# Kernel optimization log

Hardware: AMD Instinct MI355X
Metric: run time of the kernel (lower is better)

Reference implementation:

```python
import jax, jax.numpy as jnp
import numpy as np

N, E = 100000, 1600000
IN, HID, NCLS = 128, 128, 64


def setup_inputs() -> dict:
    key = jax.random.key(0)
    ks = jax.random.split(key, 8)
    x = jax.random.normal(ks[0], (N, IN), jnp.float32)
    edge_index = jax.random.randint(ks[1], (2, E), 0, N, dtype=jnp.int32)
    s1 = 1.0 / np.sqrt(IN)
    s2 = 1.0 / np.sqrt(HID)
    return {
        "x": x,
        "edge_index": edge_index,
        "Wl1": jax.random.uniform(ks[2], (IN, HID), jnp.float32, -s1, s1),
        "Wr1": jax.random.uniform(ks[3], (IN, HID), jnp.float32, -s1, s1),
        "b1": jnp.zeros((HID,), jnp.float32),
        "Wl2": jax.random.uniform(ks[4], (HID, NCLS), jnp.float32, -s2, s2),
        "Wr2": jax.random.uniform(ks[5], (HID, NCLS), jnp.float32, -s2, s2),
        "b2": jnp.zeros((NCLS,), jnp.float32),
    }


def _sage_conv(x, src, dst, inv_deg, Wl, Wr, b):
    # mean-aggregate neighbor features at each destination node (PyG SAGEConv)
    agg = jax.ops.segment_sum(x[src], dst, num_segments=N)  # [N, d]
    agg = agg * inv_deg[:, None]
    # out = lin_l(mean_j x_j) + lin_r(x_i); bias lives in lin_l
    return agg @ Wl + x @ Wr + b


def reference(x, edge_index, Wl1, Wr1, b1, Wl2, Wr2, b2):
    src, dst = edge_index[0], edge_index[1]
    deg = jax.ops.segment_sum(jnp.ones((E,), jnp.float32), dst, num_segments=N)
    inv_deg = 1.0 / jnp.maximum(deg, 1.0)
    h = _sage_conv(x, src, dst, inv_deg, Wl1, Wr1, b1)
    h = jax.nn.relu(h)
    # dropout is identity at inference (training=False)
    h = _sage_conv(h, src, dst, inv_deg, Wl2, Wr2, b2)
    return jax.nn.log_softmax(h, axis=1)
```

## Files before the change

kernel.cpp:

```cpp
#include <hip/hip_runtime.h>
#include <hip/hip_bf16.h>


typedef __attribute__((ext_vector_type(8))) short short8;
typedef __attribute__((ext_vector_type(4))) float f32x4;
typedef __attribute__((ext_vector_type(2))) float f32x2;

#define NPB 512
#define BCAP 16384
#define CHUNK 8192

__device__ __forceinline__ ushort f2bf(float f) {
    unsigned u = __float_as_uint(f);
    return (ushort)((u + 0x7fff + ((u >> 16) & 1)) >> 16);
}
__device__ __forceinline__ float bflo(unsigned v) { return __uint_as_float(v << 16); }
__device__ __forceinline__ float bfhi(unsigned v) { return __uint_as_float(v & 0xffff0000u); }
__device__ __forceinline__ unsigned pk4bf(float a, float b) {
    return (unsigned)f2bf(a) | ((unsigned)f2bf(b) << 16);
}

__global__ void bucket_scatter(const int* __restrict__ src, const int* __restrict__ dst,
                               int* __restrict__ bcount, unsigned* __restrict__ bbuf,
                               int E, int NB) {
    __shared__ unsigned entry[CHUNK];
    __shared__ unsigned char ebkt[CHUNK];
    __shared__ int lhist[256], lbase[256], lcur[256];
    int tid = threadIdx.x;
    lhist[tid] = 0;
    __syncthreads();
    int e0 = blockIdx.x * CHUNK;
    int cnt = min(CHUNK, E - e0);
    int nv = cnt >> 2;
    for (int t = tid; t < nv; t += 256) {
        int4 d4 = ((const int4*)(dst + e0))[t];
        int4 s4 = ((const int4*)(src + e0))[t];
        int i = t * 4;
        int b0 = d4.x >> 9, b1 = d4.y >> 9, b2 = d4.z >> 9, b3 = d4.w >> 9;
        entry[i + 0] = ((unsigned)s4.x << 9) | (unsigned)(d4.x & 511);
        entry[i + 1] = ((unsigned)s4.y << 9) | (unsigned)(d4.y & 511);
        entry[i + 2] = ((unsigned)s4.z << 9) | (unsigned)(d4.z & 511);
        entry[i + 3] = ((unsigned)s4.w << 9) | (unsigned)(d4.w & 511);
        ebkt[i + 0] = (unsigned char)b0; ebkt[i + 1] = (unsigned char)b1;
        ebkt[i + 2] = (unsigned char)b2; ebkt[i + 3] = (unsigned char)b3;
        atomicAdd(&lhist[b0], 1); atomicAdd(&lhist[b1], 1);
        atomicAdd(&lhist[b2], 1); atomicAdd(&lhist[b3], 1);
    }
    for (int i = (nv << 2) + tid; i < cnt; i += 256) {
        int d = dst[e0 + i], s = src[e0 + i];
        int b = d >> 9;
        entry[i] = ((unsigned)s << 9) | (unsigned)(d & 511);
        ebkt[i] = (unsigned char)b;
        atomicAdd(&lhist[b], 1);
    }
    __syncthreads();
    int h = lhist[tid];
    lbase[tid] = (h > 0) ? atomicAdd(&bcount[tid], h) : 0;
    lcur[tid] = 0;
    __syncthreads();
    for (int i = tid; i < cnt; i += 256) {
        int b = ebkt[i];
        int o = atomicAdd(&lcur[b], 1);
        bbuf[(long)b * BCAP + lbase[b] + o] = entry[i];
    }
}

__global__ void scan_buckets(const int* __restrict__ bcount, int* __restrict__ bbase, int NB) {
    __shared__ int s[256];
    int tid = threadIdx.x;
    int v = (tid < NB) ? bcount[tid] : 0;
    s[tid] = v;
    __syncthreads();
    for (int off = 1; off < 256; off <<= 1) {
        int a = (tid >= off) ? s[tid - off] : 0;
        __syncthreads();
        s[tid] += a;
        __syncthreads();
    }
    if (tid < NB) bbase[tid] = s[tid] - v;
}

__global__ void build_csr(const unsigned* __restrict__ bbuf, const int* __restrict__ bcount,
                          const int* __restrict__ bbase, int* __restrict__ row_start,
                          int* __restrict__ degw, float* __restrict__ inv_deg,
                          int* __restrict__ ssrc, int N) {
    __shared__ int sdeg[NPB], lcur[NPB];
    int b = blockIdx.x, tid = threadIdx.x;
    int node0 = b * NPB;
    sdeg[tid] = 0; sdeg[tid + 256] = 0;
    __syncthreads();
    int cnt = bcount[b];
    long base = (long)b * BCAP;
    for (int i = tid; i < cnt; i += 256)
        atomicAdd(&sdeg[bbuf[base + i] & 511], 1);
    __syncthreads();
    int c0 = sdeg[tid], c1 = sdeg[tid + 256];
    for (int off = 1; off < NPB; off <<= 1) {
        int a0 = (tid >= off) ? sdeg[tid - off] : 0;
        int a1 = (tid + 256 >= off) ? sdeg[tid + 256 - off] : 0;
        __syncthreads();
        sdeg[tid] += a0; sdeg[tid + 256] += a1;
        __syncthreads();
    }
    int bb = bbase[b];
    int rs0 = bb + sdeg[tid] - c0;
    int rs1 = bb + sdeg[tid + 256] - c1;
    lcur[tid] = rs0; lcur[tid + 256] = rs1;
    if (node0 + tid < N) {
        row_start[node0 + tid] = rs0;
        degw[node0 + tid] = c0;
        inv_deg[node0 + tid] = 1.0f / (float)(c0 > 1 ? c0 : 1);
    }
    if (node0 + tid + 256 < N) {
        row_start[node0 + tid + 256] = rs1;
        degw[node0 + tid + 256] = c1;
        inv_deg[node0 + tid + 256] = 1.0f / (float)(c1 > 1 ? c1 : 1);
    }
    __syncthreads();
    for (int i = tid; i < cnt; i += 256) {
        unsigned w = bbuf[base + i];
        int pos = atomicAdd(&lcur[w & 511], 1);
        ssrc[pos] = (int)(w >> 9);
    }
}

__device__ __forceinline__ void wfrag_one(const float* W, ushort* Wf, int i, int COLS) {
    int j = i & 7, m = (i >> 3) & 15, kc = (i >> 7) & 15, ct = i >> 11;
    Wf[i] = f2bf(W[(kc * 8 + j) * COLS + ct * 16 + m]);
}
__global__ void cvt_w_kernel(const float* __restrict__ Wl1, const float* __restrict__ Wr1,
                             const float* __restrict__ Wl2, const float* __restrict__ Wr2,
                             ushort* __restrict__ Wf_l1, ushort* __restrict__ Wf_r1,
                             ushort* __restrict__ Wf_l2, ushort* __restrict__ Wf_r2) {
    int i = blockIdx.x * blockDim.x + threadIdx.x;
    if (i < 16384)       wfrag_one(Wl1, Wf_l1, i, 128);
    else if (i < 32768)  wfrag_one(Wr1, Wf_r1, i - 16384, 128);
    else if (i < 40960)  wfrag_one(Wl2, Wf_l2, i - 32768, 64);
    else if (i < 49152)  wfrag_one(Wr2, Wf_r2, i - 40960, 64);
}

template <int COLS, bool F32IN>
__global__ void proj_kernel(const void* __restrict__ xin,
                            const ushort* __restrict__ Wfl, const ushort* __restrict__ Wfr,
                            const float* __restrict__ bias,
                            unsigned char* __restrict__ p8,
                            ushort* __restrict__ q,
                            int N) {
    constexpr int CT = COLS / 16;
    int wave = threadIdx.x >> 6, lane = threadIdx.x & 63;
    int quad = lane >> 4, m = lane & 15;
    long row0 = (long)blockIdx.x * 64 + wave * 16;
    long node = row0 + m;
    long arow = (node < N) ? node : (N - 1);

    f32x4 accp[CT], accq[CT];
#pragma unroll
    for (int ct = 0; ct < CT; ++ct) { accp[ct] = (f32x4)0.0f; accq[ct] = (f32x4)0.0f; }

#pragma unroll
    for (int kk = 0; kk < 128; kk += 32) {
        short8 b;
        if (F32IN) {
            const float* xf = (const float*)xin + arow * 128 + kk + quad * 8;
            float4 f0 = *(const float4*)xf;
            float4 f1 = *(const float4*)(xf + 4);
            b[0] = (short)f2bf(f0.x); b[1] = (short)f2bf(f0.y);
            b[2] = (short)f2bf(f0.z); b[3] = (short)f2bf(f0.w);
            b[4] = (short)f2bf(f1.x); b[5] = (short)f2bf(f1.y);
            b[6] = (short)f2bf(f1.z); b[7] = (short)f2bf(f1.w);
        } else {
            b = *(const short8*)((const ushort*)xin + arow * 128 + kk + quad * 8);
        }
        int kc = (kk >> 3) + quad;
#pragma unroll
        for (int ct = 0; ct < CT; ++ct) {
            long boff = (((long)(ct * 16 + kc) * 16) + m) * 8;
            short8 al = *(const short8*)(Wfl + boff);
            short8 ar = *(const short8*)(Wfr + boff);
            accp[ct] = __builtin_amdgcn_mfma_f32_16x16x32_bf16(al, b, accp[ct], 0, 0, 0);
            accq[ct] = __builtin_amdgcn_mfma_f32_16x16x32_bf16(ar, b, accq[ct], 0, 0, 0);
        }
    }

    if (node < N) {
#pragma unroll
        for (int ct = 0; ct < CT; ++ct) {
            int c0 = ct * 16 + quad * 4;
            float4 bv = *(const float4*)(bias + c0);
            float q0 = accq[ct][0] + bv.x, q1 = accq[ct][1] + bv.y;
            float q2 = accq[ct][2] + bv.z, q3 = accq[ct][3] + bv.w;
            unsigned w = (unsigned)__builtin_amdgcn_cvt_pk_fp8_f32(accp[ct][0], accp[ct][1], 0, false);
            w = (unsigned)__builtin_amdgcn_cvt_pk_fp8_f32(accp[ct][2], accp[ct][3], (int)w, true);
            *(unsigned*)(p8 + node * COLS + c0) = w;
            uint2 qw; qw.x = pk4bf(q0, q1); qw.y = pk4bf(q2, q3);
            *(uint2*)(q + node * COLS + c0) = qw;
        }
    }
}

__global__ void agg_relu_kernel(const unsigned char* __restrict__ p8,
                                const ushort* __restrict__ q,
                                const int* __restrict__ ssrc,
                                const int* __restrict__ row_start,
                                const int* __restrict__ deg,
                                const float* __restrict__ inv_deg,
                                ushort* __restrict__ hb, int N) {
    int wave = threadIdx.x >> 6, lane = threadIdx.x & 63;
    int n = blockIdx.x * 4 + wave;
    if (n >= N) return;
    int g = lane >> 4, lm = lane & 15;
    int start = row_start[n], d = deg[n];
    const int* sp = ssrc + start;
    const unsigned char* pb = p8 + lm * 8;
    float a[8] = {};
    int j = 0;
    for (; j + 16 <= d; j += 16) {
        int s0 = sp[j + g], s1 = sp[j + 4 + g], s2 = sp[j + 8 + g], s3 = sp[j + 12 + g];
        uint2 v0 = *(const uint2*)(pb + (long)s0 * 128);
        uint2 v1 = *(const uint2*)(pb + (long)s1 * 128);
        uint2 v2 = *(const uint2*)(pb + (long)s2 * 128);
        uint2 v3 = *(const uint2*)(pb + (long)s3 * 128);
#pragma unroll
        for (int t = 0; t < 4; ++t) {
            uint2 vv = (t == 0) ? v0 : (t == 1) ? v1 : (t == 2) ? v2 : v3;
            f32x2 c0 = __builtin_amdgcn_cvt_pk_f32_fp8((int)vv.x, false);
            f32x2 c1 = __builtin_amdgcn_cvt_pk_f32_fp8((int)vv.x, true);
            f32x2 c2 = __builtin_amdgcn_cvt_pk_f32_fp8((int)vv.y, false);
            f32x2 c3 = __builtin_amdgcn_cvt_pk_f32_fp8((int)vv.y, true);
            a[0] += c0[0]; a[1] += c0[1]; a[2] += c1[0]; a[3] += c1[1];
            a[4] += c2[0]; a[5] += c2[1]; a[6] += c3[0]; a[7] += c3[1];
        }
    }
    for (; j < d; j += 4) {
        int idx = j + g;
        int s = sp[idx < d ? idx : j];
        uint2 vv = *(const uint2*)(pb + (long)s * 128);
        if (idx < d) {
            f32x2 c0 = __builtin_amdgcn_cvt_pk_f32_fp8((int)vv.x, false);
            f32x2 c1 = __builtin_amdgcn_cvt_pk_f32_fp8((int)vv.x, true);
            f32x2 c2 = __builtin_amdgcn_cvt_pk_f32_fp8((int)vv.y, false);
            f32x2 c3 = __builtin_amdgcn_cvt_pk_f32_fp8((int)vv.y, true);
            a[0] += c0[0]; a[1] += c0[1]; a[2] += c1[0]; a[3] += c1[1];
            a[4] += c2[0]; a[5] += c2[1]; a[6] += c3[0]; a[7] += c3[1];
        }
    }
#pragma unroll
    for (int t = 0; t < 8; ++t) {
        a[t] += __shfl_xor(a[t], 16);
        a[t] += __shfl_xor(a[t], 32);
    }
    if (g == 0) {
        float iv = inv_deg[n];
        uint4 qv = *(const uint4*)(q + (long)n * 128 + lm * 8);
        float h0 = fmaxf(a[0] * iv + bflo(qv.x), 0.f);
        float h1 = fmaxf(a[1] * iv + bfhi(qv.x), 0.f);
        float h2 = fmaxf(a[2] * iv + bflo(qv.y), 0.f);
        float h3 = fmaxf(a[3] * iv + bfhi(qv.y), 0.f);
        float h4 = fmaxf(a[4] * iv + bflo(qv.z), 0.f);
        float h5 = fmaxf(a[5] * iv + bfhi(qv.z), 0.f);
        float h6 = fmaxf(a[6] * iv + bflo(qv.w), 0.f);
        float h7 = fmaxf(a[7] * iv + bfhi(qv.w), 0.f);
        uint4 hw;
        hw.x = pk4bf(h0, h1); hw.y = pk4bf(h2, h3);
        hw.z = pk4bf(h4, h5); hw.w = pk4bf(h6, h7);
        *(uint4*)(hb + (long)n * 128 + lm * 8) = hw;
    }
}

__global__ void agg_lsm_kernel(const unsigned char* __restrict__ u8,
                               const ushort* __restrict__ v,
                               const int* __restrict__ ssrc,
                               const int* __restrict__ row_start,
                               const int* __restrict__ deg,
                               const float* __restrict__ inv_deg,
                               float* __restrict__ out, int N) {
    int wave = threadIdx.x >> 6, lane = threadIdx.x & 63;
    int n = blockIdx.x * 4 + wave;
    if (n >= N) return;
    int g = lane >> 3, lm = lane & 7;
    int start = row_start[n], d = deg[n];
    const int* sp = ssrc + start;
    const unsigned char* ub = u8 + lm * 8;
    float a[8] = {};
    int j = 0;
    for (; j + 16 <= d; j += 16) {
        int s0 = sp[j + g], s1 = sp[j + 8 + g];
        uint2 v0 = *(const uint2*)(ub + (long)s0 * 64);
        uint2 v1 = *(const uint2*)(ub + (long)s1 * 64);
#pragma unroll
        for (int t = 0; t < 2; ++t) {
            uint2 vv = (t == 0) ? v0 : v1;
            f32x2 c0 = __builtin_amdgcn_cvt_pk_f32_fp8((int)vv.x, false);
            f32x2 c1 = __builtin_amdgcn_cvt_pk_f32_fp8((int)vv.x, true);
            f32x2 c2 = __builtin_amdgcn_cvt_pk_f32_fp8((int)vv.y, false);
            f32x2 c3 = __builtin_amdgcn_cvt_pk_f32_fp8((int)vv.y, true);
            a[0] += c0[0]; a[1] += c0[1]; a[2] += c1[0]; a[3] += c1[1];
            a[4] += c2[0]; a[5] += c2[1]; a[6] += c3[0]; a[7] += c3[1];
        }
    }
    for (; j < d; j += 8) {
        int idx = j + g;
        int s = sp[idx < d ? idx : j];
        uint2 vv = *(const uint2*)(ub + (long)s * 64);
        if (idx < d) {
            f32x2 c0 = __builtin_amdgcn_cvt_pk_f32_fp8((int)vv.x, false);
            f32x2 c1 = __builtin_amdgcn_cvt_pk_f32_fp8((int)vv.x, true);
            f32x2 c2 = __builtin_amdgcn_cvt_pk_f32_fp8((int)vv.y, false);
            f32x2 c3 = __builtin_amdgcn_cvt_pk_f32_fp8((int)vv.y, true);
            a[0] += c0[0]; a[1] += c0[1]; a[2] += c1[0]; a[3] += c1[1];
            a[4] += c2[0]; a[5] += c2[1]; a[6] += c3[0]; a[7] += c3[1];
        }
    }
#pragma unroll
    for (int t = 0; t < 8; ++t) {
        a[t] += __shfl_xor(a[t], 8);
        a[t] += __shfl_xor(a[t], 16);
        a[t] += __shfl_xor(a[t], 32);
    }
    float iv = inv_deg[n];
    uint4 vv = *(const uint4*)(v + (long)n * 64 + lm * 8);
    float z0 = a[0] * iv + bflo(vv.x), z1 = a[1] * iv + bfhi(vv.x);
    float z2 = a[2] * iv + bflo(vv.y), z3 = a[3] * iv + bfhi(vv.y);
    float z4 = a[4] * iv + bflo(vv.z), z5 = a[5] * iv + bfhi(vv.z);
    float z6 = a[6] * iv + bflo(vv.w), z7 = a[7] * iv + bfhi(vv.w);
    float mx = fmaxf(fmaxf(fmaxf(z0, z1), fmaxf(z2, z3)),
                     fmaxf(fmaxf(z4, z5), fmaxf(z6, z7)));
#pragma unroll
    for (int o = 4; o > 0; o >>= 1) mx = fmaxf(mx, __shfl_xor(mx, o));
    float e = (__expf(z0 - mx) + __expf(z1 - mx)) + (__expf(z2 - mx) + __expf(z3 - mx)) +
              (__expf(z4 - mx) + __expf(z5 - mx)) + (__expf(z6 - mx) + __expf(z7 - mx));
#pragma unroll
    for (int o = 4; o > 0; o >>= 1) e += __shfl_xor(e, o);
    float ls = mx + __logf(e);
    if (g == 0) {
        float4 o0, o1;
        o0.x = z0 - ls; o0.y = z1 - ls; o0.z = z2 - ls; o0.w = z3 - ls;
        o1.x = z4 - ls; o1.y = z5 - ls; o1.z = z6 - ls; o1.w = z7 - ls;
        *(float4*)(out + (long)n * 64 + lm * 8) = o0;
        *(float4*)(out + (long)n * 64 + lm * 8 + 4) = o1;
    }
}

extern "C" void kernel_launch(void* const* d_in, const int* in_sizes, int n_in,
                              void* d_out, int out_size, void* d_ws, size_t ws_size,
                              hipStream_t stream) {
    const float* x   = (const float*)d_in[0];
    const int*   ei  = (const int*)d_in[1];
    const float* Wl1 = (const float*)d_in[2];
    const float* Wr1 = (const float*)d_in[3];
    const float* b1  = (const float*)d_in[4];
    const float* Wl2 = (const float*)d_in[5];
    const float* Wr2 = (const float*)d_in[6];
    const float* b2  = (const float*)d_in[7];

    const int N = in_sizes[0] / 128;
    const int E = in_sizes[1] / 2;
    const int* src = ei;
    const int* dst = ei + E;
    const int NB = (N + NPB - 1) / NPB;

    size_t off = 0;
    auto take = [&](size_t nbytes) -> void* {
        void* ptr = (void*)((char*)d_ws + off);
        off += (nbytes + 255) & ~(size_t)255;
        return ptr;
    };
    int*      bcount    = (int*)take((size_t)NB * 4);
    int*      bbase     = (int*)take((size_t)NB * 4);
    unsigned* bbuf      = (unsigned*)take((size_t)NB * BCAP * 4);
    int*      row_start = (int*)take((size_t)N * 4);
    int*      degw      = (int*)take((size_t)N * 4);
    float*    inv_deg   = (float*)take((size_t)N * 4);
    int*      ssrc      = (int*)take((size_t)E * 4);
    unsigned char* p8   = (unsigned char*)take((size_t)N * 128);
    ushort*   q         = (ushort*)take((size_t)N * 128 * 2);
    ushort*   hb        = (ushort*)take((size_t)N * 128 * 2);
    ushort*   Wf_l1     = (ushort*)take(128 * 128 * 2);
    ushort*   Wf_r1     = (ushort*)take(128 * 128 * 2);
    ushort*   Wf_l2     = (ushort*)take(64 * 128 * 2);
    ushort*   Wf_r2     = (ushort*)take(64 * 128 * 2);
    unsigned char* u8 = p8;
    ushort*        v  = q;
    (void)ws_size; (void)n_in; (void)out_size;

    hipMemsetAsync(bcount, 0, (size_t)NB * 4, stream);

    bucket_scatter<<<(E + CHUNK - 1) / CHUNK, 256, 0, stream>>>(src, dst, bcount, bbuf, E, NB);
    scan_buckets  <<<1, 256, 0, stream>>>(bcount, bbase, NB);
    build_csr     <<<NB, 256, 0, stream>>>(bbuf, bcount, bbase, row_start, degw, inv_deg, ssrc, N);
    cvt_w_kernel  <<<192, 256, 0, stream>>>(Wl1, Wr1, Wl2, Wr2, Wf_l1, Wf_r1, Wf_l2, Wf_r2);

    proj_kernel<128, true><<<(N + 63) / 64, 256, 0, stream>>>(x, Wf_l1, Wf_r1, b1, p8, q, N);
    agg_relu_kernel<<<(N + 3) / 4, 256, 0, stream>>>(p8, q, ssrc, row_start, degw, inv_deg, hb, N);

    proj_kernel<64, false><<<(N + 63) / 64, 256, 0, stream>>>(hb, Wf_l2, Wf_r2, b2, u8, v, N);
    agg_lsm_kernel<<<(N + 3) / 4, 256, 0, stream>>>(u8, v, ssrc, row_start, degw, inv_deg,
                                                    (float*)d_out, N);
}
```

Before: 297.5 us.

## Fuse edge bucketing with layer-1 projection and CSR build with aggregation

Edge bucket scattering and the layer-1 projection now run in one launch, split by block index. CSR construction is merged into the layer-1 aggregation kernel: each block sorts its bucket in LDS and aggregates straight from shared memory. The sorted sources are written back in place into bbuf, which removes the separate scan, the ssrc array and two launches. Buckets shrink to 128 nodes with a fixed capacity of 3072, so edges beyond that capacity would be silently dropped. Accumulators switch to packed f32x2 adds.

```diff
diff --git a/kernel.cpp b/kernel.cpp
--- a/kernel.cpp
+++ b/kernel.cpp
@@ -6,9 +6,10 @@
 typedef __attribute__((ext_vector_type(4))) float f32x4;
 typedef __attribute__((ext_vector_type(2))) float f32x2;
 
-#define NPB 512
-#define BCAP 16384
+#define NPB 128
+#define BCAP 3072
 #define CHUNK 8192
+#define MAXNB 1024
 
 __device__ __forceinline__ ushort f2bf(float f) {
     unsigned u = __float_as_uint(f);
@@ -19,109 +20,8 @@
 __device__ __forceinline__ unsigned pk4bf(float a, float b) {
     return (unsigned)f2bf(a) | ((unsigned)f2bf(b) << 16);
 }
-
-__global__ void bucket_scatter(const int* __restrict__ src, const int* __restrict__ dst,
-                               int* __restrict__ bcount, unsigned* __restrict__ bbuf,
-                               int E, int NB) {
-    __shared__ unsigned entry[CHUNK];
-    __shared__ unsigned char ebkt[CHUNK];
-    __shared__ int lhist[256], lbase[256], lcur[256];
-    int tid = threadIdx.x;
-    lhist[tid] = 0;
-    __syncthreads();
-    int e0 = blockIdx.x * CHUNK;
-    int cnt = min(CHUNK, E - e0);
-    int nv = cnt >> 2;
-    for (int t = tid; t < nv; t += 256) {
-        int4 d4 = ((const int4*)(dst + e0))[t];
-        int4 s4 = ((const int4*)(src + e0))[t];
-        int i = t * 4;
-        int b0 = d4.x >> 9, b1 = d4.y >> 9, b2 = d4.z >> 9, b3 = d4.w >> 9;
-        entry[i + 0] = ((unsigned)s4.x << 9) | (unsigned)(d4.x & 511);
-        entry[i + 1] = ((unsigned)s4.y << 9) | (unsigned)(d4.y & 511);
-        entry[i + 2] = ((unsigned)s4.z << 9) | (unsigned)(d4.z & 511);
-        entry[i + 3] = ((unsigned)s4.w << 9) | (unsigned)(d4.w & 511);
-        ebkt[i + 0] = (unsigned char)b0; ebkt[i + 1] = (unsigned char)b1;
-        ebkt[i + 2] = (unsigned char)b2; ebkt[i + 3] = (unsigned char)b3;
-        atomicAdd(&lhist[b0], 1); atomicAdd(&lhist[b1], 1);
-        atomicAdd(&lhist[b2], 1); atomicAdd(&lhist[b3], 1);
-    }
-    for (int i = (nv << 2) + tid; i < cnt; i += 256) {
-        int d = dst[e0 + i], s = src[e0 + i];
-        int b = d >> 9;
-        entry[i] = ((unsigned)s << 9) | (unsigned)(d & 511);
-        ebkt[i] = (unsigned char)b;
-        atomicAdd(&lhist[b], 1);
-    }
-    __syncthreads();
-    int h = lhist[tid];
-    lbase[tid] = (h > 0) ? atomicAdd(&bcount[tid], h) : 0;
-    lcur[tid] = 0;
-    __syncthreads();
-    for (int i = tid; i < cnt; i += 256) {
-        int b = ebkt[i];
-        int o = atomicAdd(&lcur[b], 1);
-        bbuf[(long)b * BCAP + lbase[b] + o] = entry[i];
-    }
-}
-
-__global__ void scan_buckets(const int* __restrict__ bcount, int* __restrict__ bbase, int NB) {
-    __shared__ int s[256];
-    int tid = threadIdx.x;
-    int v = (tid < NB) ? bcount[tid] : 0;
-    s[tid] = v;
-    __syncthreads();
-    for (int off = 1; off < 256; off <<= 1) {
-        int a = (tid >= off) ? s[tid - off] : 0;
-        __syncthreads();
-        s[tid] += a;
-        __syncthreads();
-    }
-    if (tid < NB) bbase[tid] = s[tid] - v;
-}
-
-__global__ void build_csr(const unsigned* __restrict__ bbuf, const int* __restrict__ bcount,
-                          const int* __restrict__ bbase, int* __restrict__ row_start,
-                          int* __restrict__ degw, float* __restrict__ inv_deg,
-                          int* __restrict__ ssrc, int N) {
-    __shared__ int sdeg[NPB], lcur[NPB];
-    int b = blockIdx.x, tid = threadIdx.x;
-    int node0 = b * NPB;
-    sdeg[tid] = 0; sdeg[tid + 256] = 0;
-    __syncthreads();
-    int cnt = bcount[b];
-    long base = (long)b * BCAP;
-    for (int i = tid; i < cnt; i += 256)
-        atomicAdd(&sdeg[bbuf[base + i] & 511], 1);
-    __syncthreads();
-    int c0 = sdeg[tid], c1 = sdeg[tid + 256];
-    for (int off = 1; off < NPB; off <<= 1) {
-        int a0 = (tid >= off) ? sdeg[tid - off] : 0;
-        int a1 = (tid + 256 >= off) ? sdeg[tid + 256 - off] : 0;
-        __syncthreads();
-        sdeg[tid] += a0; sdeg[tid + 256] += a1;
-        __syncthreads();
-    }
-    int bb = bbase[b];
-    int rs0 = bb + sdeg[tid] - c0;
-    int rs1 = bb + sdeg[tid + 256] - c1;
-    lcur[tid] = rs0; lcur[tid + 256] = rs1;
-    if (node0 + tid < N) {
-        row_start[node0 + tid] = rs0;
-        degw[node0 + tid] = c0;
-        inv_deg[node0 + tid] = 1.0f / (float)(c0 > 1 ? c0 : 1);
-    }
-    if (node0 + tid + 256 < N) {
-        row_start[node0 + tid + 256] = rs1;
-        degw[node0 + tid + 256] = c1;
-        inv_deg[node0 + tid + 256] = 1.0f / (float)(c1 > 1 ? c1 : 1);
-    }
-    __syncthreads();
-    for (int i = tid; i < cnt; i += 256) {
-        unsigned w = bbuf[base + i];
-        int pos = atomicAdd(&lcur[w & 511], 1);
-        ssrc[pos] = (int)(w >> 9);
-    }
+__device__ __forceinline__ f32x2 shflx2(f32x2 v, int m) {
+    f32x2 r; r[0] = __shfl_xor(v[0], m); r[1] = __shfl_xor(v[1], m); return r;
 }
 
 __device__ __forceinline__ void wfrag_one(const float* W, ushort* Wf, int i, int COLS) {
@@ -140,16 +40,15 @@
 }
 
 template <int COLS, bool F32IN>
-__global__ void proj_kernel(const void* __restrict__ xin,
+__device__ __forceinline__ void proj_body(int bid, int tid,
+                            const void* __restrict__ xin,
                             const ushort* __restrict__ Wfl, const ushort* __restrict__ Wfr,
                             const float* __restrict__ bias,
-                            unsigned char* __restrict__ p8,
-                            ushort* __restrict__ q,
-                            int N) {
+                            unsigned char* __restrict__ p8, ushort* __restrict__ q, int N) {
     constexpr int CT = COLS / 16;
-    int wave = threadIdx.x >> 6, lane = threadIdx.x & 63;
+    int wave = tid >> 6, lane = tid & 63;
     int quad = lane >> 4, m = lane & 15;
-    long row0 = (long)blockIdx.x * 64 + wave * 16;
+    long row0 = (long)bid * 64 + wave * 16;
     long node = row0 + m;
     long arow = (node < N) ? node : (N - 1);
 
@@ -198,73 +97,172 @@
     }
 }
 
-__global__ void agg_relu_kernel(const unsigned char* __restrict__ p8,
-                                const ushort* __restrict__ q,
-                                const int* __restrict__ ssrc,
-                                const int* __restrict__ row_start,
-                                const int* __restrict__ deg,
-                                const float* __restrict__ inv_deg,
-                                ushort* __restrict__ hb, int N) {
-    int wave = threadIdx.x >> 6, lane = threadIdx.x & 63;
-    int n = blockIdx.x * 4 + wave;
-    if (n >= N) return;
-    int g = lane >> 4, lm = lane & 15;
-    int start = row_start[n], d = deg[n];
-    const int* sp = ssrc + start;
+__global__ void __launch_bounds__(256)
+fused_scatter_proj1(const int* __restrict__ src, const int* __restrict__ dst,
+                    int* __restrict__ bcount, int* __restrict__ bbuf, int E, int NB, int NSC,
+                    const float* __restrict__ x,
+                    const ushort* __restrict__ Wfl, const ushort* __restrict__ Wfr,
+                    const float* __restrict__ bias,
+                    unsigned char* __restrict__ p8, ushort* __restrict__ q, int N) {
+    __shared__ int lhist[MAXNB], lbase[MAXNB], lcur[MAXNB];
+    int tid = threadIdx.x;
+    if ((int)blockIdx.x >= NSC) {
+        proj_body<128, true>((int)blockIdx.x - NSC, tid, x, Wfl, Wfr, bias, p8, q, N);
+        return;
+    }
+    for (int i = tid; i < NB; i += 256) lhist[i] = 0;
+    __syncthreads();
+    int e0 = blockIdx.x * CHUNK;
+    int cnt = min(CHUNK, E - e0);
+    int nv = cnt >> 2;
+    for (int t = tid; t < nv; t += 256) {
+        int4 d4 = ((const int4*)(dst + e0))[t];
+        atomicAdd(&lhist[d4.x >> 7], 1); atomicAdd(&lhist[d4.y >> 7], 1);
+        atomicAdd(&lhist[d4.z >> 7], 1); atomicAdd(&lhist[d4.w >> 7], 1);
+    }
+    for (int i = (nv << 2) + tid; i < cnt; i += 256)
+        atomicAdd(&lhist[dst[e0 + i] >> 7], 1);
+    __syncthreads();
+    for (int i = tid; i < NB; i += 256) {
+        int h = lhist[i];
+        lbase[i] = (h > 0) ? atomicAdd(&bcount[i], h) : 0;
+        lcur[i] = 0;
+    }
+    __syncthreads();
+    for (int t = tid; t < nv; t += 256) {
+        int4 d4 = ((const int4*)(dst + e0))[t];
+        int4 s4 = ((const int4*)(src + e0))[t];
+#pragma unroll
+        for (int j = 0; j < 4; ++j) {
+            int d = (j == 0) ? d4.x : (j == 1) ? d4.y : (j == 2) ? d4.z : d4.w;
+            int s = (j == 0) ? s4.x : (j == 1) ? s4.y : (j == 2) ? s4.z : s4.w;
+            int b = d >> 7;
+            int pos = lbase[b] + atomicAdd(&lcur[b], 1);
+            if (pos < BCAP) bbuf[(long)b * BCAP + pos] = (s << 7) | (d & 127);
+        }
+    }
+    for (int i = (nv << 2) + tid; i < cnt; i += 256) {
+        int d = dst[e0 + i], s = src[e0 + i];
+        int b = d >> 7;
+        int pos = lbase[b] + atomicAdd(&lcur[b], 1);
+        if (pos < BCAP) bbuf[(long)b * BCAP + pos] = (s << 7) | (d & 127);
+    }
+}
+
+__global__ void __launch_bounds__(256)
+csr_agg_kernel(int* __restrict__ bbuf, const int* __restrict__ bcount,
+               const unsigned char* __restrict__ p8, const ushort* __restrict__ q,
+               int* __restrict__ row_start, int* __restrict__ degw,
+               float* __restrict__ inv_deg, ushort* __restrict__ hb, int N) {
+    __shared__ int lent[BCAP];
+    __shared__ int lssrc[BCAP];
+    __shared__ int ldeg[NPB], lrs[NPB], lc[NPB];
+    int b = blockIdx.x, tid = threadIdx.x;
+    int cnt = min(bcount[b], BCAP);
+    long base = (long)b * BCAP;
+    if (tid < NPB) ldeg[tid] = 0;
+    __syncthreads();
+    for (int i = tid; i < cnt; i += 256) {
+        int e = bbuf[base + i];
+        lent[i] = e;
+        atomicAdd(&ldeg[e & 127], 1);
+    }
+    __syncthreads();
+    if (tid < NPB) lrs[tid] = ldeg[tid];
+    __syncthreads();
+    for (int off = 1; off < NPB; off <<= 1) {
+        int a = (tid < NPB && tid >= off) ? lrs[tid - off] : 0;
+        __syncthreads();
+        if (tid < NPB) lrs[tid] += a;
+        __syncthreads();
+    }
+    if (tid < NPB) {
+        int d = ldeg[tid];
+        int rs = lrs[tid] - d;
+        lrs[tid] = rs;
+        lc[tid] = rs;
+        int node = b * NPB + tid;
+        if (node < N) {
+            row_start[node] = (int)(base + rs);
+            degw[node] = d;
+            inv_deg[node] = 1.0f / (float)(d > 1 ? d : 1);
+        }
+    }
+    __syncthreads();
+    for (int i = tid; i < cnt; i += 256) {
+        int e = lent[i];
+        int pos = atomicAdd(&lc[e & 127], 1);
+        int s = e >> 7;
+        lssrc[pos] = s;
+        bbuf[base + pos] = s;
+    }
+    __syncthreads();
+
+    int wv = tid >> 6, ln = tid & 63;
+    int g = ln >> 4, lm = ln & 15;
     const unsigned char* pb = p8 + lm * 8;
-    float a[8] = {};
-    int j = 0;
-    for (; j + 16 <= d; j += 16) {
-        int s0 = sp[j + g], s1 = sp[j + 4 + g], s2 = sp[j + 8 + g], s3 = sp[j + 12 + g];
-        uint2 v0 = *(const uint2*)(pb + (long)s0 * 128);
-        uint2 v1 = *(const uint2*)(pb + (long)s1 * 128);
-        uint2 v2 = *(const uint2*)(pb + (long)s2 * 128);
-        uint2 v3 = *(const uint2*)(pb + (long)s3 * 128);
-#pragma unroll
-        for (int t = 0; t < 4; ++t) {
-            uint2 vv = (t == 0) ? v0 : (t == 1) ? v1 : (t == 2) ? v2 : v3;
-            f32x2 c0 = __builtin_amdgcn_cvt_pk_f32_fp8((int)vv.x, false);
-            f32x2 c1 = __builtin_amdgcn_cvt_pk_f32_fp8((int)vv.x, true);
-            f32x2 c2 = __builtin_amdgcn_cvt_pk_f32_fp8((int)vv.y, false);
-            f32x2 c3 = __builtin_amdgcn_cvt_pk_f32_fp8((int)vv.y, true);
-            a[0] += c0[0]; a[1] += c0[1]; a[2] += c1[0]; a[3] += c1[1];
-            a[4] += c2[0]; a[5] += c2[1]; a[6] += c3[0]; a[7] += c3[1];
-        }
-    }
-    for (; j < d; j += 4) {
-        int idx = j + g;
-        int s = sp[idx < d ? idx : j];
-        uint2 vv = *(const uint2*)(pb + (long)s * 128);
-        if (idx < d) {
-            f32x2 c0 = __builtin_amdgcn_cvt_pk_f32_fp8((int)vv.x, false);
-            f32x2 c1 = __builtin_amdgcn_cvt_pk_f32_fp8((int)vv.x, true);
-            f32x2 c2 = __builtin_amdgcn_cvt_pk_f32_fp8((int)vv.y, false);
-            f32x2 c3 = __builtin_amdgcn_cvt_pk_f32_fp8((int)vv.y, true);
-            a[0] += c0[0]; a[1] += c0[1]; a[2] += c1[0]; a[3] += c1[1];
-            a[4] += c2[0]; a[5] += c2[1]; a[6] += c3[0]; a[7] += c3[1];
-        }
-    }
-#pragma unroll
-    for (int t = 0; t < 8; ++t) {
-        a[t] += __shfl_xor(a[t], 16);
-        a[t] += __shfl_xor(a[t], 32);
-    }
-    if (g == 0) {
-        float iv = inv_deg[n];
-        uint4 qv = *(const uint4*)(q + (long)n * 128 + lm * 8);
-        float h0 = fmaxf(a[0] * iv + bflo(qv.x), 0.f);
-        float h1 = fmaxf(a[1] * iv + bfhi(qv.x), 0.f);
-        float h2 = fmaxf(a[2] * iv + bflo(qv.y), 0.f);
-        float h3 = fmaxf(a[3] * iv + bfhi(qv.y), 0.f);
-        float h4 = fmaxf(a[4] * iv + bflo(qv.z), 0.f);
-        float h5 = fmaxf(a[5] * iv + bfhi(qv.z), 0.f);
-        float h6 = fmaxf(a[6] * iv + bflo(qv.w), 0.f);
-        float h7 = fmaxf(a[7] * iv + bfhi(qv.w), 0.f);
-        uint4 hw;
-        hw.x = pk4bf(h0, h1); hw.y = pk4bf(h2, h3);
-        hw.z = pk4bf(h4, h5); hw.w = pk4bf(h6, h7);
-        *(uint4*)(hb + (long)n * 128 + lm * 8) = hw;
-    }
+    for (int nl = wv; nl < NPB; nl += 4) {
+        int node = b * NPB + nl;
+        if (node >= N) break;
+        int rs = lrs[nl], d = ldeg[nl];
+        f32x2 a0 = (f32x2)0.f, a1 = (f32x2)0.f, a2 = (f32x2)0.f, a3 = (f32x2)0.f;
+        int j = 0;
+        for (; j + 16 <= d; j += 16) {
+            int s0 = lssrc[rs + j + g],      s1 = lssrc[rs + j + 4 + g];
+            int s2 = lssrc[rs + j + 8 + g],  s3 = lssrc[rs + j + 12 + g];
+            uint2 v0 = *(const uint2*)(pb + (long)s0 * 128);
+            uint2 v1 = *(const uint2*)(pb + (long)s1 * 128);
+            uint2 v2 = *(const uint2*)(pb + (long)s2 * 128);
+            uint2 v3 = *(const uint2*)(pb + (long)s3 * 128);
+#pragma unroll
+            for (int t = 0; t < 4; ++t) {
+                uint2 vv = (t == 0) ? v0 : (t == 1) ? v1 : (t == 2) ? v2 : v3;
+                a0 += __builtin_amdgcn_cvt_pk_f32_fp8((int)vv.x, false);
+                a1 += __builtin_amdgcn_cvt_pk_f32_fp8((int)vv.x, true);
+                a2 += __builtin_amdgcn_cvt_pk_f32_fp8((int)vv.y, false);
+                a3 += __builtin_amdgcn_cvt_pk_f32_fp8((int)vv.y, true);
+            }
+        }
+        for (; j < d; j += 4) {
+            int idx = j + g;
+            int s = lssrc[rs + (idx < d ? idx : j)];
+            uint2 vv = *(const uint2*)(pb + (long)s * 128);
+            if (idx < d) {
+                a0 += __builtin_amdgcn_cvt_pk_f32_fp8((int)vv.x, false);
+                a1 += __builtin_amdgcn_cvt_pk_f32_fp8((int)vv.x, true);
+                a2 += __builtin_amdgcn_cvt_pk_f32_fp8((int)vv.y, false);
+                a3 += __builtin_amdgcn_cvt_pk_f32_fp8((int)vv.y, true);
+            }
+        }
+        a0 += shflx2(a0, 16); a1 += shflx2(a1, 16);
+        a2 += shflx2(a2, 16); a3 += shflx2(a3, 16);
+        a0 += shflx2(a0, 32); a1 += shflx2(a1, 32);
+        a2 += shflx2(a2, 32); a3 += shflx2(a3, 32);
+        if (g == 0) {
+            float iv = inv_deg[node];
+            uint4 qv = *(const uint4*)(q + (long)node * 128 + lm * 8);
+            float h0 = fmaxf(a0[0] * iv + bflo(qv.x), 0.f);
+            float h1 = fmaxf(a0[1] * iv + bfhi(qv.x), 0.f);
+            float h2 = fmaxf(a1[0] * iv + bflo(qv.y), 0.f);
+            float h3 = fmaxf(a1[1] * iv + bfhi(qv.y), 0.f);
+            float h4 = fmaxf(a2[0] * iv + bflo(qv.z), 0.f);
+            float h5 = fmaxf(a2[1] * iv + bfhi(qv.z), 0.f);
+            float h6 = fmaxf(a3[0] * iv + bflo(qv.w), 0.f);
+            float h7 = fmaxf(a3[1] * iv + bfhi(qv.w), 0.f);
+            uint4 hw;
+            hw.x = pk4bf(h0, h1); hw.y = pk4bf(h2, h3);
+            hw.z = pk4bf(h4, h5); hw.w = pk4bf(h6, h7);
+            *(uint4*)(hb + (long)node * 128 + lm * 8) = hw;
+        }
+    }
+}
+
+__global__ void __launch_bounds__(256)
+proj2_kernel(const ushort* __restrict__ hb,
+             const ushort* __restrict__ Wfl, const ushort* __restrict__ Wfr,
+             const float* __restrict__ bias,
+             unsigned char* __restrict__ u8, ushort* __restrict__ v, int N) {
+    proj_body<64, false>((int)blockIdx.x, (int)threadIdx.x, hb, Wfl, Wfr, bias, u8, v, N);
 }
 
 __global__ void agg_lsm_kernel(const unsigned char* __restrict__ u8,
@@ -281,7 +279,7 @@
     int start = row_start[n], d = deg[n];
     const int* sp = ssrc + start;
     const unsigned char* ub = u8 + lm * 8;
-    float a[8] = {};
+    f32x2 a0 = (f32x2)0.f, a1 = (f32x2)0.f, a2 = (f32x2)0.f, a3 = (f32x2)0.f;
     int j = 0;
     for (; j + 16 <= d; j += 16) {
         int s0 = sp[j + g], s1 = sp[j + 8 + g];
@@ -290,12 +288,10 @@
 #pragma unroll
         for (int t = 0; t < 2; ++t) {
             uint2 vv = (t == 0) ? v0 : v1;
-            f32x2 c0 = __builtin_amdgcn_cvt_pk_f32_fp8((int)vv.x, false);
-            f32x2 c1 = __builtin_amdgcn_cvt_pk_f32_fp8((int)vv.x, true);
-            f32x2 c2 = __builtin_amdgcn_cvt_pk_f32_fp8((int)vv.y, false);
-            f32x2 c3 = __builtin_amdgcn_cvt_pk_f32_fp8((int)vv.y, true);
-            a[0] += c0[0]; a[1] += c0[1]; a[2] += c1[0]; a[3] += c1[1];
-            a[4] += c2[0]; a[5] += c2[1]; a[6] += c3[0]; a[7] += c3[1];
+            a0 += __builtin_amdgcn_cvt_pk_f32_fp8((int)vv.x, false);
+            a1 += __builtin_amdgcn_cvt_pk_f32_fp8((int)vv.x, true);
+            a2 += __builtin_amdgcn_cvt_pk_f32_fp8((int)vv.y, false);
+            a3 += __builtin_amdgcn_cvt_pk_f32_fp8((int)vv.y, true);
         }
     }
     for (; j < d; j += 8) {
@@ -303,26 +299,22 @@
         int s = sp[idx < d ? idx : j];
         uint2 vv = *(const uint2*)(ub + (long)s * 64);
         if (idx < d) {
-            f32x2 c0 = __builtin_amdgcn_cvt_pk_f32_fp8((int)vv.x, false);
-            f32x2 c1 = __builtin_amdgcn_cvt_pk_f32_fp8((int)vv.x, true);
-            f32x2 c2 = __builtin_amdgcn_cvt_pk_f32_fp8((int)vv.y, false);
-            f32x2 c3 = __builtin_amdgcn_cvt_pk_f32_fp8((int)vv.y, true);
-            a[0] += c0[0]; a[1] += c0[1]; a[2] += c1[0]; a[3] += c1[1];
-            a[4] += c2[0]; a[5] += c2[1]; a[6] += c3[0]; a[7] += c3[1];
-        }
-    }
-#pragma unroll
-    for (int t = 0; t < 8; ++t) {
-        a[t] += __shfl_xor(a[t], 8);
-        a[t] += __shfl_xor(a[t], 16);
-        a[t] += __shfl_xor(a[t], 32);
-    }
+            a0 += __builtin_amdgcn_cvt_pk_f32_fp8((int)vv.x, false);
+            a1 += __builtin_amdgcn_cvt_pk_f32_fp8((int)vv.x, true);
+            a2 += __builtin_amdgcn_cvt_pk_f32_fp8((int)vv.y, false);
+            a3 += __builtin_amdgcn_cvt_pk_f32_fp8((int)vv.y, true);
+        }
+    }
+    a0 += shflx2(a0, 8);  a1 += shflx2(a1, 8);  a2 += shflx2(a2, 8);  a3 += shflx2(a3, 8);
+    a0 += shflx2(a0, 16); a1 += shflx2(a1, 16); a2 += shflx2(a2, 16); a3 += shflx2(a3, 16);
+    a0 += shflx2(a0, 32); a1 += shflx2(a1, 32); a2 += shflx2(a2, 32); a3 += shflx2(a3, 32);
+
     float iv = inv_deg[n];
     uint4 vv = *(const uint4*)(v + (long)n * 64 + lm * 8);
-    float z0 = a[0] * iv + bflo(vv.x), z1 = a[1] * iv + bfhi(vv.x);
-    float z2 = a[2] * iv + bflo(vv.y), z3 = a[3] * iv + bfhi(vv.y);
-    float z4 = a[4] * iv + bflo(vv.z), z5 = a[5] * iv + bfhi(vv.z);
-    float z6 = a[6] * iv + bflo(vv.w), z7 = a[7] * iv + bfhi(vv.w);
+    float z0 = a0[0] * iv + bflo(vv.x), z1 = a0[1] * iv + bfhi(vv.x);
+    float z2 = a1[0] * iv + bflo(vv.y), z3 = a1[1] * iv + bfhi(vv.y);
+    float z4 = a2[0] * iv + bflo(vv.z), z5 = a2[1] * iv + bfhi(vv.z);
+    float z6 = a3[0] * iv + bflo(vv.w), z7 = a3[1] * iv + bfhi(vv.w);
     float mx = fmaxf(fmaxf(fmaxf(z0, z1), fmaxf(z2, z3)),
                      fmaxf(fmaxf(z4, z5), fmaxf(z6, z7)));
 #pragma unroll
@@ -358,6 +350,7 @@
     const int* src = ei;
     const int* dst = ei + E;
     const int NB = (N + NPB - 1) / NPB;
+    const int NSC = (E + CHUNK - 1) / CHUNK;
 
     size_t off = 0;
     auto take = [&](size_t nbytes) -> void* {
@@ -366,12 +359,10 @@
         return ptr;
     };
     int*      bcount    = (int*)take((size_t)NB * 4);
-    int*      bbase     = (int*)take((size_t)NB * 4);
-    unsigned* bbuf      = (unsigned*)take((size_t)NB * BCAP * 4);
+    int*      bbuf      = (int*)take((size_t)NB * BCAP * 4);
     int*      row_start = (int*)take((size_t)N * 4);
     int*      degw      = (int*)take((size_t)N * 4);
     float*    inv_deg   = (float*)take((size_t)N * 4);
-    int*      ssrc      = (int*)take((size_t)E * 4);
     unsigned char* p8   = (unsigned char*)take((size_t)N * 128);
     ushort*   q         = (ushort*)take((size_t)N * 128 * 2);
     ushort*   hb        = (ushort*)take((size_t)N * 128 * 2);
@@ -385,15 +376,15 @@
 
     hipMemsetAsync(bcount, 0, (size_t)NB * 4, stream);
 
-    bucket_scatter<<<(E + CHUNK - 1) / CHUNK, 256, 0, stream>>>(src, dst, bcount, bbuf, E, NB);
-    scan_buckets  <<<1, 256, 0, stream>>>(bcount, bbase, NB);
-    build_csr     <<<NB, 256, 0, stream>>>(bbuf, bcount, bbase, row_start, degw, inv_deg, ssrc, N);
-    cvt_w_kernel  <<<192, 256, 0, stream>>>(Wl1, Wr1, Wl2, Wr2, Wf_l1, Wf_r1, Wf_l2, Wf_r2);
-
-    proj_kernel<128, true><<<(N + 63) / 64, 256, 0, stream>>>(x, Wf_l1, Wf_r1, b1, p8, q, N);
-    agg_relu_kernel<<<(N + 3) / 4, 256, 0, stream>>>(p8, q, ssrc, row_start, degw, inv_deg, hb, N);
-
-    proj_kernel<64, false><<<(N + 63) / 64, 256, 0, stream>>>(hb, Wf_l2, Wf_r2, b2, u8, v, N);
-    agg_lsm_kernel<<<(N + 3) / 4, 256, 0, stream>>>(u8, v, ssrc, row_start, degw, inv_deg,
-                                                    (float*)d_out, N);
-}
+    cvt_w_kernel<<<192, 256, 0, stream>>>(Wl1, Wr1, Wl2, Wr2, Wf_l1, Wf_r1, Wf_l2, Wf_r2);
+
+    int P1 = (N + 63) / 64;
+    fused_scatter_proj1<<<NSC + P1, 256, 0, stream>>>(src, dst, bcount, bbuf, E, NB, NSC,
+                                                      x, Wf_l1, Wf_r1, b1, p8, q, N);
+
+    csr_agg_kernel<<<NB, 256, 0, stream>>>(bbuf, bcount, p8, q, row_start, degw, inv_deg, hb, N);
+
+    proj2_kernel<<<(N + 63) / 64, 256, 0, stream>>>(hb, Wf_l2, Wf_r2, b2, u8, v, N);
+    agg_lsm_kernel<<<(N + 3) / 4, 256, 0, stream>>>(u8, v, (const int*)bbuf, row_start, degw,
+                                                    inv_deg, (float*)d_out, N);
+}
```

After: 301.2 us. Within noise of the previous version (+1.3%).
